# Optimization experiments

Hardware: AMD Instinct MI355X
Metric: run time of the kernel (lower is better)

Reference implementation:

```python
import jax, jax.numpy as jnp
import numpy as np

D_MODEL = 512
NHEAD = 8
HEAD_DIM = D_MODEL // NHEAD
LN_EPS = 1e-5


def setup_inputs() -> dict:
    key = jax.random.key(0)
    ks = jax.random.split(key, 6)
    S, B, D = 2048, 64, D_MODEL
    src = jax.random.normal(ks[0], (S, B, D), dtype=jnp.float32)
    seq_lengths = jax.random.randint(ks[1], (B,), 1, S + 1, dtype=jnp.int32)
    sc = 1.0 / np.sqrt(D)
    in_proj_weight = jax.random.normal(ks[2], (3 * D, D), dtype=jnp.float32) * sc
    in_proj_bias = jnp.zeros((3 * D,), dtype=jnp.float32)
    out_proj_weight = jax.random.normal(ks[3], (D, D), dtype=jnp.float32) * sc
    out_proj_bias = jnp.zeros((D,), dtype=jnp.float32)
    ln_weight = jnp.ones((D,), dtype=jnp.float32)
    ln_bias = jnp.zeros((D,), dtype=jnp.float32)
    return {
        'src': src, 'seq_lengths': seq_lengths,
        'in_proj_weight': in_proj_weight, 'in_proj_bias': in_proj_bias,
        'out_proj_weight': out_proj_weight, 'out_proj_bias': out_proj_bias,
        'ln_weight': ln_weight, 'ln_bias': ln_bias,
    }


def reference(src, seq_lengths, in_proj_weight, in_proj_bias,
              out_proj_weight, out_proj_bias, ln_weight, ln_bias):
    S, B, D = src.shape
    H, hd = NHEAD, HEAD_DIM
    # gather last valid token per batch element -> queries [B, D]
    q_in = src[seq_lengths - 1, jnp.arange(B)]
    Wq, Wk, Wv = in_proj_weight[:D], in_proj_weight[D:2 * D], in_proj_weight[2 * D:]
    bq, bk, bv = in_proj_bias[:D], in_proj_bias[D:2 * D], in_proj_bias[2 * D:]
    scale = 1.0 / jnp.sqrt(jnp.asarray(hd, src.dtype))
    q = (q_in @ Wq.T + bq).reshape(B, H, hd) * scale          # [B,H,hd]
    k = (src @ Wk.T + bk).reshape(S, B, H, hd)                # [S,B,H,hd]
    v = (src @ Wv.T + bv).reshape(S, B, H, hd)
    scores = jnp.einsum('bhd,sbhd->bhs', q, k)                # [B,H,S]
    attn = jax.nn.softmax(scores, axis=-1)
    ctx = jnp.einsum('bhs,sbhd->bhd', attn, v).reshape(B, D)  # [B,D]
    attn_out = ctx @ out_proj_weight.T + out_proj_bias        # [B,D]
    # residual: attn_out broadcasts across the sequence dim (src2 is [1,B,D])
    x = src + attn_out[None, :, :]
    mu = jnp.mean(x, axis=-1, keepdims=True)
    var = jnp.mean(jnp.square(x - mu), axis=-1, keepdims=True)
    return (x - mu) / jnp.sqrt(var + LN_EPS) * ln_weight + ln_bias
```

## Files before the change

kernel.cpp:

```cpp
#include <hip/hip_runtime.h>
#include <hip/hip_bf16.h>

#define S_LEN 2048
#define BATCH 64
#define DMODEL 512
#define NHEAD 8
#define HDIM 64
#define LN_EPS_F 1e-5f
#define QSCALE 0.125f

__global__ void __launch_bounds__(256) k_q_qk(
    const float* __restrict__ src, const int* __restrict__ seqlen,
    const float* __restrict__ w_in, const float* __restrict__ b_in,
    float* __restrict__ qk)
{
    __shared__ float xl[DMODEL];
    __shared__ float ql[DMODEL];
    const int b = blockIdx.x;
    const int t = threadIdx.x;
    const int last = seqlen[b] - 1;
    const float* xrow = src + ((size_t)last * BATCH + b) * DMODEL;
    for (int i = t; i < DMODEL; i += 256) xl[i] = xrow[i];
    __syncthreads();
    for (int d = t; d < DMODEL; d += 256) {
        const float* wr = w_in + (size_t)d * DMODEL;
        float acc = b_in[d];
        for (int i = 0; i < DMODEL; i += 4) {
            const float4 r = *reinterpret_cast<const float4*>(wr + i);
            acc += r.x * xl[i] + r.y * xl[i + 1] + r.z * xl[i + 2] + r.w * xl[i + 3];
        }
        ql[d] = acc * QSCALE;
    }
    __syncthreads();
    for (int h = 0; h < NHEAD; h++) {
        for (int dp = t; dp < DMODEL; dp += 256) {
            float acc = 0.f;
#pragma unroll 8
            for (int j = 0; j < HDIM; j++) {
                acc += w_in[((size_t)(DMODEL + h * HDIM + j)) * DMODEL + dp] * ql[h * HDIM + j];
            }
            qk[((size_t)b * NHEAD + h) * DMODEL + dp] = acc;
        }
    }
}

__global__ void __launch_bounds__(256) k_scores(
    const float* __restrict__ src, const float* __restrict__ qk,
    float* __restrict__ scores)
{
    const int b = blockIdx.x;
    const int sb = blockIdx.y;
    const int t = threadIdx.x;
    const int wave = t >> 6, lane = t & 63;

    float qr[NHEAD][8];
    const float* qb = qk + (size_t)b * NHEAD * DMODEL;
#pragma unroll
    for (int h = 0; h < NHEAD; h++) {
        const float4 a = *reinterpret_cast<const float4*>(qb + h * DMODEL + lane * 8);
        const float4 c = *reinterpret_cast<const float4*>(qb + h * DMODEL + lane * 8 + 4);
        qr[h][0] = a.x; qr[h][1] = a.y; qr[h][2] = a.z; qr[h][3] = a.w;
        qr[h][4] = c.x; qr[h][5] = c.y; qr[h][6] = c.z; qr[h][7] = c.w;
    }
#pragma unroll
    for (int i = 0; i < 8; i++) {
        const int s = sb * 32 + wave * 8 + i;
        const float* xrow = src + ((size_t)s * BATCH + b) * DMODEL + lane * 8;
        const float4 xa = *reinterpret_cast<const float4*>(xrow);
        const float4 xc = *reinterpret_cast<const float4*>(xrow + 4);
        float xf[8];
        xf[0] = xa.x; xf[1] = xa.y; xf[2] = xa.z; xf[3] = xa.w;
        xf[4] = xc.x; xf[5] = xc.y; xf[6] = xc.z; xf[7] = xc.w;
        float p[NHEAD];
#pragma unroll
        for (int h = 0; h < NHEAD; h++) {
            float a = 0.f;
#pragma unroll
            for (int j = 0; j < 8; j++) a += qr[h][j] * xf[j];
            p[h] = a;
        }
#pragma unroll
        for (int off = 32; off; off >>= 1) {
#pragma unroll
            for (int h = 0; h < NHEAD; h++) p[h] += __shfl_down(p[h], off, 64);
        }
        if (lane == 0) {
#pragma unroll
            for (int h = 0; h < NHEAD; h++)
                scores[((size_t)b * NHEAD + h) * S_LEN + s] = p[h];
        }
    }
}

__global__ void __launch_bounds__(256) k_softmax(float* __restrict__ scores)
{
    const int bh = blockIdx.x;
    const int t = threadIdx.x;
    float* p = scores + (size_t)bh * S_LEN;
    float v[8];
    float m = -1e30f;
#pragma unroll
    for (int k = 0; k < 8; k++) { v[k] = p[t + k * 256]; m = fmaxf(m, v[k]); }
    __shared__ float red[256];
    red[t] = m; __syncthreads();
    for (int o = 128; o; o >>= 1) { if (t < o) red[t] = fmaxf(red[t], red[t + o]); __syncthreads(); }
    m = red[0];
    __syncthreads();
    float s = 0.f;
#pragma unroll
    for (int k = 0; k < 8; k++) { v[k] = __expf(v[k] - m); s += v[k]; }
    red[t] = s; __syncthreads();
    for (int o = 128; o; o >>= 1) { if (t < o) red[t] += red[t + o]; __syncthreads(); }
    const float inv = 1.0f / red[0];
#pragma unroll
    for (int k = 0; k < 8; k++) p[t + k * 256] = v[k] * inv;
}

__global__ void __launch_bounds__(256) k_xbar(
    const float* __restrict__ src, const float* __restrict__ attn,
    float* __restrict__ xpart)
{
    __shared__ float al[NHEAD][256];
    const int b = blockIdx.x;
    const int c = blockIdx.y;
    const int t = threadIdx.x;
    const int s0 = c * 256;
#pragma unroll
    for (int h = 0; h < NHEAD; h++)
        al[h][t] = attn[((size_t)b * NHEAD + h) * S_LEN + s0 + t];
    __syncthreads();
    float acc0[NHEAD] = {0.f, 0.f, 0.f, 0.f, 0.f, 0.f, 0.f, 0.f};
    float acc1[NHEAD] = {0.f, 0.f, 0.f, 0.f, 0.f, 0.f, 0.f, 0.f};
    const float* base = src + (size_t)s0 * BATCH * DMODEL + (size_t)b * DMODEL + 2 * t;
#pragma unroll 4
    for (int i = 0; i < 256; i++) {
        const float2 xv = *reinterpret_cast<const float2*>(base + (size_t)i * BATCH * DMODEL);
#pragma unroll
        for (int h = 0; h < NHEAD; h++) {
            const float a = al[h][i];
            acc0[h] += a * xv.x;
            acc1[h] += a * xv.y;
        }
    }
#pragma unroll
    for (int h = 0; h < NHEAD; h++) {
        const size_t idx = (((size_t)c * BATCH + b) * NHEAD + h) * DMODEL + 2 * t;
        *reinterpret_cast<float2*>(xpart + idx) = make_float2(acc0[h], acc1[h]);
    }
}

__global__ void __launch_bounds__(256) k_ctx_proj(
    const float* __restrict__ xpart, const float* __restrict__ w_in,
    const float* __restrict__ b_in, const float* __restrict__ w_out,
    const float* __restrict__ b_out, float* __restrict__ attn_out)
{
    __shared__ float xb[NHEAD * DMODEL];
    __shared__ float ctx[DMODEL];
    const int b = blockIdx.x;
    const int t = threadIdx.x;
    for (int i = t; i < NHEAD * DMODEL; i += 256) {
        float a = 0.f;
#pragma unroll
        for (int c = 0; c < 8; c++)
            a += xpart[(((size_t)c * BATCH + b) * NHEAD) * DMODEL + i];
        xb[i] = a;
    }
    __syncthreads();
    for (int e = t; e < DMODEL; e += 256) {
        const int h = e >> 6;
        const float* wr = w_in + ((size_t)(2 * DMODEL + e)) * DMODEL;
        float acc = b_in[2 * DMODEL + e];
        const float* xr = &xb[h * DMODEL];
        for (int d = 0; d < DMODEL; d += 4) {
            const float4 r = *reinterpret_cast<const float4*>(wr + d);
            acc += r.x * xr[d] + r.y * xr[d + 1] + r.z * xr[d + 2] + r.w * xr[d + 3];
        }
        ctx[e] = acc;
    }
    __syncthreads();
    for (int o = t; o < DMODEL; o += 256) {
        const float* wr = w_out + (size_t)o * DMODEL;
        float acc = b_out[o];
        for (int e = 0; e < DMODEL; e += 4) {
            const float4 r = *reinterpret_cast<const float4*>(wr + e);
            acc += r.x * ctx[e] + r.y * ctx[e + 1] + r.z * ctx[e + 2] + r.w * ctx[e + 3];
        }
        attn_out[(size_t)b * DMODEL + o] = acc;
    }
}

__global__ void __launch_bounds__(256) k_ln(
    const float* __restrict__ src, const float* __restrict__ attn_out,
    const float* __restrict__ g, const float* __restrict__ beta,
    float* __restrict__ out)
{
    const int row = blockIdx.x;
    const int b = row & (BATCH - 1);
    const int t = threadIdx.x;
    const float2 xv = *(reinterpret_cast<const float2*>(src + (size_t)row * DMODEL) + t);
    const float2 ao = *reinterpret_cast<const float2*>(attn_out + (size_t)b * DMODEL + 2 * t);
    const float x0 = xv.x + ao.x;
    const float x1 = xv.y + ao.y;
    __shared__ float rs[256], rq[256];
    rs[t] = x0 + x1;
    rq[t] = x0 * x0 + x1 * x1;
    __syncthreads();
    for (int o = 128; o; o >>= 1) {
        if (t < o) { rs[t] += rs[t + o]; rq[t] += rq[t + o]; }
        __syncthreads();
    }
    const float mu = rs[0] * (1.0f / DMODEL);
    const float var = rq[0] * (1.0f / DMODEL) - mu * mu;
    const float inv = rsqrtf(var + LN_EPS_F);
    const float y0 = (x0 - mu) * inv * g[2 * t] + beta[2 * t];
    const float y1 = (x1 - mu) * inv * g[2 * t + 1] + beta[2 * t + 1];
    *reinterpret_cast<float2*>(out + (size_t)row * DMODEL + 2 * t) = make_float2(y0, y1);
}

extern "C" void kernel_launch(void* const* d_in, const int* in_sizes, int n_in,
                              void* d_out, int out_size, void* d_ws, size_t ws_size,
                              hipStream_t stream)
{
    const float* src   = (const float*)d_in[0];
    const int*   slen  = (const int*)d_in[1];
    const float* w_in  = (const float*)d_in[2];
    const float* b_in  = (const float*)d_in[3];
    const float* w_out = (const float*)d_in[4];
    const float* b_out = (const float*)d_in[5];
    const float* g     = (const float*)d_in[6];
    const float* beta  = (const float*)d_in[7];
    float* out = (float*)d_out;

    char* ws = (char*)d_ws;
    float* qk       = (float*)(ws);
    float* scores   = (float*)(ws + (1u << 20));
    float* xpart    = (float*)(ws + 5u * (1u << 20));
    float* attn_out = (float*)(ws + 13u * (1u << 20));

    k_q_qk<<<BATCH, 256, 0, stream>>>(src, slen, w_in, b_in, qk);
    k_scores<<<dim3(BATCH, S_LEN / 32), 256, 0, stream>>>(src, qk, scores);
    k_softmax<<<BATCH * NHEAD, 256, 0, stream>>>(scores);
    k_xbar<<<dim3(BATCH, 8), 256, 0, stream>>>(src, scores, xpart);
    k_ctx_proj<<<BATCH, 256, 0, stream>>>(xpart, w_in, b_in, w_out, b_out, attn_out);
    k_ln<<<S_LEN * BATCH, 256, 0, stream>>>(src, attn_out, g, beta, out);
}
```

Measured before the change: 776.1 us.

## Rework all stages: wave-level reductions, split small GEMV kernels, one-row-per-wave LayerNorm

Several kernels change at once. The q/qk and ctx projection kernels get a second grid dimension, and ctx/out-projection are split into two kernels for more parallelism. The scores kernel replaces its per-row shuffle reduction with a transposing butterfly reduction so every lane writes one score. Softmax and LayerNorm switch to wave shuffle reductions, and LayerNorm processes one row per wave with float4 accesses instead of a 256-thread block per row. The xbar kernel stores attention weights as [s][h] so it can read them with float4 LDS loads. The costs are higher register pressure in the scores kernel (64 accumulators) and one extra kernel launch.

```diff
diff --git a/kernel.cpp b/kernel.cpp
--- a/kernel.cpp
+++ b/kernel.cpp
@@ -1,5 +1,4 @@
 #include <hip/hip_runtime.h>
-#include <hip/hip_bf16.h>
 
 #define S_LEN 2048
 #define BATCH 64
@@ -15,32 +14,35 @@
     float* __restrict__ qk)
 {
     __shared__ float xl[DMODEL];
-    __shared__ float ql[DMODEL];
-    const int b = blockIdx.x;
+    __shared__ float ql[256];
+    const int b = blockIdx.x;
+    const int y = blockIdx.y;
     const int t = threadIdx.x;
     const int last = seqlen[b] - 1;
     const float* xrow = src + ((size_t)last * BATCH + b) * DMODEL;
     for (int i = t; i < DMODEL; i += 256) xl[i] = xrow[i];
     __syncthreads();
-    for (int d = t; d < DMODEL; d += 256) {
+    {
+        const int d = y * 256 + t;
         const float* wr = w_in + (size_t)d * DMODEL;
         float acc = b_in[d];
         for (int i = 0; i < DMODEL; i += 4) {
             const float4 r = *reinterpret_cast<const float4*>(wr + i);
             acc += r.x * xl[i] + r.y * xl[i + 1] + r.z * xl[i + 2] + r.w * xl[i + 3];
         }
-        ql[d] = acc * QSCALE;
-    }
-    __syncthreads();
-    for (int h = 0; h < NHEAD; h++) {
-        for (int dp = t; dp < DMODEL; dp += 256) {
-            float acc = 0.f;
-#pragma unroll 8
-            for (int j = 0; j < HDIM; j++) {
-                acc += w_in[((size_t)(DMODEL + h * HDIM + j)) * DMODEL + dp] * ql[h * HDIM + j];
-            }
-            qk[((size_t)b * NHEAD + h) * DMODEL + dp] = acc;
-        }
+        ql[t] = acc * QSCALE;
+    }
+    __syncthreads();
+#pragma unroll
+    for (int r = 0; r < 8; r++) {
+        const int hl = r >> 1;
+        const int dp = (r & 1) * 256 + t;
+        const int h = y * 4 + hl;
+        float acc = 0.f;
+#pragma unroll 16
+        for (int j = 0; j < HDIM; j++)
+            acc += w_in[((size_t)(DMODEL + h * HDIM + j)) * DMODEL + dp] * ql[hl * HDIM + j];
+        qk[((size_t)b * NHEAD + h) * DMODEL + dp] = acc;
     }
 }
 
@@ -54,64 +56,73 @@
     const int wave = t >> 6, lane = t & 63;
 
     float qr[NHEAD][8];
-    const float* qb = qk + (size_t)b * NHEAD * DMODEL;
+    const float* qb = qk + (size_t)b * NHEAD * DMODEL + lane * 8;
 #pragma unroll
     for (int h = 0; h < NHEAD; h++) {
-        const float4 a = *reinterpret_cast<const float4*>(qb + h * DMODEL + lane * 8);
-        const float4 c = *reinterpret_cast<const float4*>(qb + h * DMODEL + lane * 8 + 4);
+        const float4 a = *reinterpret_cast<const float4*>(qb + h * DMODEL);
+        const float4 c = *reinterpret_cast<const float4*>(qb + h * DMODEL + 4);
         qr[h][0] = a.x; qr[h][1] = a.y; qr[h][2] = a.z; qr[h][3] = a.w;
         qr[h][4] = c.x; qr[h][5] = c.y; qr[h][6] = c.z; qr[h][7] = c.w;
     }
+    const int sbase = sb * 32 + wave * 8;
+    float acc[64];
+#pragma unroll
+    for (int j = 0; j < 64; j++) acc[j] = 0.f;
 #pragma unroll
     for (int i = 0; i < 8; i++) {
-        const int s = sb * 32 + wave * 8 + i;
-        const float* xrow = src + ((size_t)s * BATCH + b) * DMODEL + lane * 8;
+        const float* xrow = src + ((size_t)(sbase + i) * BATCH + b) * DMODEL + lane * 8;
         const float4 xa = *reinterpret_cast<const float4*>(xrow);
         const float4 xc = *reinterpret_cast<const float4*>(xrow + 4);
         float xf[8];
         xf[0] = xa.x; xf[1] = xa.y; xf[2] = xa.z; xf[3] = xa.w;
         xf[4] = xc.x; xf[5] = xc.y; xf[6] = xc.z; xf[7] = xc.w;
-        float p[NHEAD];
 #pragma unroll
         for (int h = 0; h < NHEAD; h++) {
-            float a = 0.f;
+            float a = acc[h * 8 + i];
 #pragma unroll
             for (int j = 0; j < 8; j++) a += qr[h][j] * xf[j];
-            p[h] = a;
+            acc[h * 8 + i] = a;
         }
-#pragma unroll
-        for (int off = 32; off; off >>= 1) {
-#pragma unroll
-            for (int h = 0; h < NHEAD; h++) p[h] += __shfl_down(p[h], off, 64);
+    }
+#pragma unroll
+    for (int st = 0; st < 6; st++) {
+        const int m = 32 >> st;
+        const int nh = 32 >> st;
+        const bool hi = (lane & m) != 0;
+#pragma unroll
+        for (int j = 0; j < nh; j++) {
+            const float keep = hi ? acc[j + nh] : acc[j];
+            const float give = hi ? acc[j] : acc[j + nh];
+            acc[j] = keep + __shfl_xor(give, m, 64);
         }
-        if (lane == 0) {
-#pragma unroll
-            for (int h = 0; h < NHEAD; h++)
-                scores[((size_t)b * NHEAD + h) * S_LEN + s] = p[h];
-        }
-    }
+    }
+    scores[((size_t)b * NHEAD + (lane >> 3)) * S_LEN + sbase + (lane & 7)] = acc[0];
 }
 
 __global__ void __launch_bounds__(256) k_softmax(float* __restrict__ scores)
 {
     const int bh = blockIdx.x;
     const int t = threadIdx.x;
+    const int wave = t >> 6, lane = t & 63;
     float* p = scores + (size_t)bh * S_LEN;
     float v[8];
     float m = -1e30f;
 #pragma unroll
     for (int k = 0; k < 8; k++) { v[k] = p[t + k * 256]; m = fmaxf(m, v[k]); }
-    __shared__ float red[256];
-    red[t] = m; __syncthreads();
-    for (int o = 128; o; o >>= 1) { if (t < o) red[t] = fmaxf(red[t], red[t + o]); __syncthreads(); }
-    m = red[0];
-    __syncthreads();
+#pragma unroll
+    for (int mk = 32; mk; mk >>= 1) m = fmaxf(m, __shfl_xor(m, mk, 64));
+    __shared__ float redm[4], reds[4];
+    if (lane == 0) redm[wave] = m;
+    __syncthreads();
+    m = fmaxf(fmaxf(redm[0], redm[1]), fmaxf(redm[2], redm[3]));
     float s = 0.f;
 #pragma unroll
     for (int k = 0; k < 8; k++) { v[k] = __expf(v[k] - m); s += v[k]; }
-    red[t] = s; __syncthreads();
-    for (int o = 128; o; o >>= 1) { if (t < o) red[t] += red[t + o]; __syncthreads(); }
-    const float inv = 1.0f / red[0];
+#pragma unroll
+    for (int mk = 32; mk; mk >>= 1) s += __shfl_xor(s, mk, 64);
+    if (lane == 0) reds[wave] = s;
+    __syncthreads();
+    const float inv = 1.0f / (reds[0] + reds[1] + reds[2] + reds[3]);
 #pragma unroll
     for (int k = 0; k < 8; k++) p[t + k * 256] = v[k] * inv;
 }
@@ -120,14 +131,19 @@
     const float* __restrict__ src, const float* __restrict__ attn,
     float* __restrict__ xpart)
 {
-    __shared__ float al[NHEAD][256];
+    __shared__ float al[256][8];
     const int b = blockIdx.x;
     const int c = blockIdx.y;
     const int t = threadIdx.x;
     const int s0 = c * 256;
-#pragma unroll
-    for (int h = 0; h < NHEAD; h++)
-        al[h][t] = attn[((size_t)b * NHEAD + h) * S_LEN + s0 + t];
+    {
+        float v[8];
+#pragma unroll
+        for (int h = 0; h < NHEAD; h++)
+            v[h] = attn[((size_t)b * NHEAD + h) * S_LEN + s0 + t];
+        *reinterpret_cast<float4*>(&al[t][0]) = make_float4(v[0], v[1], v[2], v[3]);
+        *reinterpret_cast<float4*>(&al[t][4]) = make_float4(v[4], v[5], v[6], v[7]);
+    }
     __syncthreads();
     float acc0[NHEAD] = {0.f, 0.f, 0.f, 0.f, 0.f, 0.f, 0.f, 0.f};
     float acc1[NHEAD] = {0.f, 0.f, 0.f, 0.f, 0.f, 0.f, 0.f, 0.f};
@@ -135,12 +151,16 @@
 #pragma unroll 4
     for (int i = 0; i < 256; i++) {
         const float2 xv = *reinterpret_cast<const float2*>(base + (size_t)i * BATCH * DMODEL);
-#pragma unroll
-        for (int h = 0; h < NHEAD; h++) {
-            const float a = al[h][i];
-            acc0[h] += a * xv.x;
-            acc1[h] += a * xv.y;
-        }
+        const float4 a0 = *reinterpret_cast<const float4*>(&al[i][0]);
+        const float4 a1 = *reinterpret_cast<const float4*>(&al[i][4]);
+        acc0[0] += a0.x * xv.x; acc1[0] += a0.x * xv.y;
+        acc0[1] += a0.y * xv.x; acc1[1] += a0.y * xv.y;
+        acc0[2] += a0.z * xv.x; acc1[2] += a0.z * xv.y;
+        acc0[3] += a0.w * xv.x; acc1[3] += a0.w * xv.y;
+        acc0[4] += a1.x * xv.x; acc1[4] += a1.x * xv.y;
+        acc0[5] += a1.y * xv.x; acc1[5] += a1.y * xv.y;
+        acc0[6] += a1.z * xv.x; acc1[6] += a1.z * xv.y;
+        acc0[7] += a1.w * xv.x; acc1[7] += a1.w * xv.y;
     }
 #pragma unroll
     for (int h = 0; h < NHEAD; h++) {
@@ -149,44 +169,52 @@
     }
 }
 
-__global__ void __launch_bounds__(256) k_ctx_proj(
+__global__ void __launch_bounds__(256) k_ctx(
     const float* __restrict__ xpart, const float* __restrict__ w_in,
-    const float* __restrict__ b_in, const float* __restrict__ w_out,
+    const float* __restrict__ b_in, float* __restrict__ ctx)
+{
+    __shared__ float xb[4 * DMODEL];
+    const int b = blockIdx.x;
+    const int y = blockIdx.y;
+    const int t = threadIdx.x;
+    for (int i = t; i < 4 * DMODEL; i += 256) {
+        float a = 0.f;
+#pragma unroll
+        for (int c = 0; c < 8; c++)
+            a += xpart[((size_t)c * BATCH + b) * (NHEAD * DMODEL) + y * 4 * DMODEL + i];
+        xb[i] = a;
+    }
+    __syncthreads();
+    const int e = y * 256 + t;
+    const int hl = t >> 6;
+    const float* wr = w_in + ((size_t)(2 * DMODEL + e)) * DMODEL;
+    const float* xr = &xb[hl * DMODEL];
+    float acc = b_in[2 * DMODEL + e];
+    for (int d = 0; d < DMODEL; d += 4) {
+        const float4 r = *reinterpret_cast<const float4*>(wr + d);
+        acc += r.x * xr[d] + r.y * xr[d + 1] + r.z * xr[d + 2] + r.w * xr[d + 3];
+    }
+    ctx[(size_t)b * DMODEL + e] = acc;
+}
+
+__global__ void __launch_bounds__(256) k_outproj(
+    const float* __restrict__ ctx, const float* __restrict__ w_out,
     const float* __restrict__ b_out, float* __restrict__ attn_out)
 {
-    __shared__ float xb[NHEAD * DMODEL];
-    __shared__ float ctx[DMODEL];
-    const int b = blockIdx.x;
-    const int t = threadIdx.x;
-    for (int i = t; i < NHEAD * DMODEL; i += 256) {
-        float a = 0.f;
-#pragma unroll
-        for (int c = 0; c < 8; c++)
-            a += xpart[(((size_t)c * BATCH + b) * NHEAD) * DMODEL + i];
-        xb[i] = a;
-    }
-    __syncthreads();
-    for (int e = t; e < DMODEL; e += 256) {
-        const int h = e >> 6;
-        const float* wr = w_in + ((size_t)(2 * DMODEL + e)) * DMODEL;
-        float acc = b_in[2 * DMODEL + e];
-        const float* xr = &xb[h * DMODEL];
-        for (int d = 0; d < DMODEL; d += 4) {
-            const float4 r = *reinterpret_cast<const float4*>(wr + d);
-            acc += r.x * xr[d] + r.y * xr[d + 1] + r.z * xr[d + 2] + r.w * xr[d + 3];
-        }
-        ctx[e] = acc;
-    }
-    __syncthreads();
-    for (int o = t; o < DMODEL; o += 256) {
-        const float* wr = w_out + (size_t)o * DMODEL;
-        float acc = b_out[o];
-        for (int e = 0; e < DMODEL; e += 4) {
-            const float4 r = *reinterpret_cast<const float4*>(wr + e);
-            acc += r.x * ctx[e] + r.y * ctx[e + 1] + r.z * ctx[e + 2] + r.w * ctx[e + 3];
-        }
-        attn_out[(size_t)b * DMODEL + o] = acc;
-    }
+    __shared__ float cl[DMODEL];
+    const int b = blockIdx.x;
+    const int y = blockIdx.y;
+    const int t = threadIdx.x;
+    for (int i = t; i < DMODEL; i += 256) cl[i] = ctx[(size_t)b * DMODEL + i];
+    __syncthreads();
+    const int o = y * 256 + t;
+    const float* wr = w_out + (size_t)o * DMODEL;
+    float acc = b_out[o];
+    for (int e = 0; e < DMODEL; e += 4) {
+        const float4 r = *reinterpret_cast<const float4*>(wr + e);
+        acc += r.x * cl[e] + r.y * cl[e + 1] + r.z * cl[e + 2] + r.w * cl[e + 3];
+    }
+    attn_out[(size_t)b * DMODEL + o] = acc;
 }
 
 __global__ void __launch_bounds__(256) k_ln(
@@ -194,27 +222,47 @@
     const float* __restrict__ g, const float* __restrict__ beta,
     float* __restrict__ out)
 {
-    const int row = blockIdx.x;
+    const int t = threadIdx.x;
+    const int wave = t >> 6, lane = t & 63;
+    const int row = blockIdx.x * 4 + wave;
     const int b = row & (BATCH - 1);
-    const int t = threadIdx.x;
-    const float2 xv = *(reinterpret_cast<const float2*>(src + (size_t)row * DMODEL) + t);
-    const float2 ao = *reinterpret_cast<const float2*>(attn_out + (size_t)b * DMODEL + 2 * t);
-    const float x0 = xv.x + ao.x;
-    const float x1 = xv.y + ao.y;
-    __shared__ float rs[256], rq[256];
-    rs[t] = x0 + x1;
-    rq[t] = x0 * x0 + x1 * x1;
-    __syncthreads();
-    for (int o = 128; o; o >>= 1) {
-        if (t < o) { rs[t] += rs[t + o]; rq[t] += rq[t + o]; }
-        __syncthreads();
-    }
-    const float mu = rs[0] * (1.0f / DMODEL);
-    const float var = rq[0] * (1.0f / DMODEL) - mu * mu;
+    const int d0 = lane * 8;
+    const float* xp = src + (size_t)row * DMODEL + d0;
+    const float4 xa = *reinterpret_cast<const float4*>(xp);
+    const float4 xc = *reinterpret_cast<const float4*>(xp + 4);
+    const float* ap = attn_out + (size_t)b * DMODEL + d0;
+    const float4 aa = *reinterpret_cast<const float4*>(ap);
+    const float4 ac = *reinterpret_cast<const float4*>(ap + 4);
+    float x[8];
+    x[0] = xa.x + aa.x; x[1] = xa.y + aa.y; x[2] = xa.z + aa.z; x[3] = xa.w + aa.w;
+    x[4] = xc.x + ac.x; x[5] = xc.y + ac.y; x[6] = xc.z + ac.z; x[7] = xc.w + ac.w;
+    float s1 = 0.f, s2 = 0.f;
+#pragma unroll
+    for (int j = 0; j < 8; j++) { s1 += x[j]; s2 += x[j] * x[j]; }
+#pragma unroll
+    for (int m = 32; m; m >>= 1) {
+        s1 += __shfl_xor(s1, m, 64);
+        s2 += __shfl_xor(s2, m, 64);
+    }
+    const float mu = s1 * (1.0f / DMODEL);
+    const float var = s2 * (1.0f / DMODEL) - mu * mu;
     const float inv = rsqrtf(var + LN_EPS_F);
-    const float y0 = (x0 - mu) * inv * g[2 * t] + beta[2 * t];
-    const float y1 = (x1 - mu) * inv * g[2 * t + 1] + beta[2 * t + 1];
-    *reinterpret_cast<float2*>(out + (size_t)row * DMODEL + 2 * t) = make_float2(y0, y1);
+    const float4 ga = *reinterpret_cast<const float4*>(g + d0);
+    const float4 gc = *reinterpret_cast<const float4*>(g + d0 + 4);
+    const float4 ba = *reinterpret_cast<const float4*>(beta + d0);
+    const float4 bc = *reinterpret_cast<const float4*>(beta + d0 + 4);
+    float4 y0, y1;
+    y0.x = (x[0] - mu) * inv * ga.x + ba.x;
+    y0.y = (x[1] - mu) * inv * ga.y + ba.y;
+    y0.z = (x[2] - mu) * inv * ga.z + ba.z;
+    y0.w = (x[3] - mu) * inv * ga.w + ba.w;
+    y1.x = (x[4] - mu) * inv * gc.x + bc.x;
+    y1.y = (x[5] - mu) * inv * gc.y + bc.y;
+    y1.z = (x[6] - mu) * inv * gc.z + bc.z;
+    y1.w = (x[7] - mu) * inv * gc.w + bc.w;
+    float* op = out + (size_t)row * DMODEL + d0;
+    *reinterpret_cast<float4*>(op) = y0;
+    *reinterpret_cast<float4*>(op + 4) = y1;
 }
 
 extern "C" void kernel_launch(void* const* d_in, const int* in_sizes, int n_in,
@@ -236,11 +284,13 @@
     float* scores   = (float*)(ws + (1u << 20));
     float* xpart    = (float*)(ws + 5u * (1u << 20));
     float* attn_out = (float*)(ws + 13u * (1u << 20));
-
-    k_q_qk<<<BATCH, 256, 0, stream>>>(src, slen, w_in, b_in, qk);
+    float* ctxbuf   = (float*)(ws + 13u * (1u << 20) + (1u << 17));
+
+    k_q_qk<<<dim3(BATCH, 2), 256, 0, stream>>>(src, slen, w_in, b_in, qk);
     k_scores<<<dim3(BATCH, S_LEN / 32), 256, 0, stream>>>(src, qk, scores);
     k_softmax<<<BATCH * NHEAD, 256, 0, stream>>>(scores);
     k_xbar<<<dim3(BATCH, 8), 256, 0, stream>>>(src, scores, xpart);
-    k_ctx_proj<<<BATCH, 256, 0, stream>>>(xpart, w_in, b_in, w_out, b_out, attn_out);
-    k_ln<<<S_LEN * BATCH, 256, 0, stream>>>(src, attn_out, g, beta, out);
-}
+    k_ctx<<<dim3(BATCH, 2), 256, 0, stream>>>(xpart, w_in, b_in, ctxbuf);
+    k_outproj<<<dim3(BATCH, 2), 256, 0, stream>>>(ctxbuf, w_out, b_out, attn_out);
+    k_ln<<<S_LEN * BATCH / 4, 256, 0, stream>>>(src, attn_out, g, beta, out);
+}
```

Measured after the change: 661.2 us. 14.8% less time.
